# Performance work log

Measured on AMD Instinct MI355X. Metric: run time of the kernel, lower is better.

Reference implementation:

```python
import jax, jax.numpy as jnp
import numpy as np

B, S, E, H, L, NQ, FFN, V, C = 16, 2048, 256, 4, 2, 8, 512, 50257, 2
DK = E // H  # wires per attention head


def _pos_encoding(seq_len, dim):
    pos = jnp.arange(seq_len, dtype=jnp.float32)[:, None]
    div = jnp.exp(jnp.arange(0, dim, 2, dtype=jnp.float32) * (-np.log(10000.0) / dim))
    pe = jnp.zeros((seq_len, dim), dtype=jnp.float32)
    pe = pe.at[:, 0::2].set(jnp.sin(pos * div))
    pe = pe.at[:, 1::2].set(jnp.cos(pos * div))
    return pe


def _layernorm(x, g, b, eps=1e-5):
    m = x.mean(-1, keepdims=True)
    v = ((x - m) ** 2).mean(-1, keepdims=True)
    return (x - m) / jnp.sqrt(v + eps) * g + b


def setup_inputs() -> dict:
    key = jax.random.key(0)
    ks = jax.random.split(key, 9)
    f = lambda k, shape, s: jax.random.normal(k, shape, dtype=jnp.float32) * s
    return {
        "tokens": jax.random.randint(ks[0], (B, S), 0, V),
        "embed": f(ks[1], (V, E), 0.02),
        "attn_theta": f(ks[2], (L, DK), 1.0),
        "combine_w": f(ks[3], (L, E, E), 0.05),
        "combine_b": jnp.zeros((L, E), jnp.float32),
        "ffn_theta": f(ks[4], (L, NQ), 1.0),
        "lin1_w": f(ks[5], (L, NQ, FFN), 0.1),
        "lin1_b": jnp.zeros((L, FFN), jnp.float32),
        "lin2_w": f(ks[6], (L, FFN, E), 0.05),
        "lin2_b": jnp.zeros((L, E), jnp.float32),
        "ln1_g": jnp.ones((L, E), jnp.float32),
        "ln1_b": jnp.zeros((L, E), jnp.float32),
        "ln2_g": jnp.ones((L, E), jnp.float32),
        "ln2_b": jnp.zeros((L, E), jnp.float32),
        "cls_w": f(ks[7], (E, C), 0.05),
        "cls_b": jnp.zeros((C,), jnp.float32),
    }


def reference(tokens, embed, attn_theta, combine_w, combine_b, ffn_theta,
              lin1_w, lin1_b, lin2_w, lin2_b, ln1_g, ln1_b, ln2_g, ln2_b,
              cls_w, cls_b):
    # token embedding + sinusoidal positional encoding
    x = embed[tokens] + _pos_encoding(S, E)[None]  # [B,S,E]
    for l in range(L):
        # QuantumAttention: per-head RX-encode(x) then trainable RX(theta),
        # PauliZ expectation => cos(x + theta); same theta shared across heads,
        # head split/merge preserves feature layout => tile theta over heads.
        theta = jnp.tile(attn_theta[l], H)  # [E]
        attn = jnp.einsum('bse,ef->bsf', jnp.cos(x + theta), combine_w[l]) + combine_b[l]
        x = _layernorm(x + attn, ln1_g[l], ln1_b[l])
        # FeedForwardQuantum: RX-encode first NQ features, trainable RY(theta),
        # PauliZ expectation => cos(x) * cos(theta)
        q = jnp.cos(x[..., :NQ]) * jnp.cos(ffn_theta[l])  # [B,S,NQ]
        h = jax.nn.relu(jnp.einsum('bsn,nf->bsf', q, lin1_w[l]) + lin1_b[l])
        ffn = jnp.einsum('bsf,fe->bse', h, lin2_w[l]) + lin2_b[l]
        x = _layernorm(x + ffn, ln2_g[l], ln2_b[l])
    pooled = x.mean(axis=1)  # [B,E]
    return pooled @ cls_w + cls_b  # [B,C] logits
```

## Files before the change

kernel.cpp:

```cpp
#include <hip/hip_runtime.h>
#include <cstdint>
#include <cstddef>

#define SEQ   2048
#define EDIM  256
#define NBATCH 16
#define XLD   264

typedef unsigned short u16;
typedef __attribute__((ext_vector_type(8))) __bf16 bf16x8;
typedef __attribute__((ext_vector_type(4))) float f32x4;

__device__ __forceinline__ float bf2f(u16 u) {
  union { unsigned int w; float f; } v; v.w = ((unsigned int)u) << 16; return v.f;
}
__device__ __forceinline__ u16 f2bf(float f) {
  union { float f; unsigned int w; } v; v.f = f;
  unsigned int r = v.w + 0x7fffu + ((v.w >> 16) & 1u);
  return (u16)(r >> 16);
}
__device__ __forceinline__ unsigned int pk2(float lo, float hi) {
  unsigned int d;
  asm("v_cvt_pk_bf16_f32 %0, %1, %2" : "=v"(d) : "v"(lo), "v"(hi));
  return d;
}
__device__ __forceinline__ float fast_cos(float x) {
  float r = x * 0.15915494309189535f;
  r = r - floorf(r);
  return __builtin_amdgcn_cosf(r);
}
__device__ __forceinline__ void unpack8(bf16x8 v, float* o) {
  const u16* p = (const u16*)&v;
  #pragma unroll
  for (int j = 0; j < 8; ++j) o[j] = bf2f(p[j]);
}

__global__ void sniff_kernel(const void* embed, int* flag) {
  int t = threadIdx.x;
  const u16* p = (const u16*)embed;
  int c = 0;
  #pragma unroll
  for (int j = 0; j < 8; ++j) {
    u16 v = p[t * 8 + j];
    int e = (v >> 7) & 0xff;
    c += (e > 128) ? 1 : 0;
  }
  #pragma unroll
  for (int d = 1; d < 64; d <<= 1) c += __shfl_xor(c, d);
  if (t == 0) *flag = (c > 64) ? 1 : 0;
}

struct CanonArgs { const void* p[11]; };

__global__ void canon_kernel(CanonArgs a, const int* __restrict__ flag,
                             u16* __restrict__ dst, float* __restrict__ divt) {
  const int off[12] = {0, 128, 640, 656, 1680, 2192, 2704, 3216, 3728, 4240, 4752, 4754};
  int i = blockIdx.x * 256 + threadIdx.x;
  if (i < 128) {
    const float c0 = 9.210340371976184f / 128.f;
    const float inv2pi = 0.15915494309189535f;
    divt[i] = __expf(-(float)i * c0) * inv2pi;
  }
  if (i >= 4754) return;
  int isf32 = *flag;
  int s = 0;
  #pragma unroll
  for (int k = 0; k < 10; ++k) s += (i >= off[k + 1]) ? 1 : 0;
  int j = i - off[s];
  dst[i] = isf32 ? f2bf(((const float*)a.p[s])[j]) : ((const u16*)a.p[s])[j];
}

__global__ void prep_kernel(const void* __restrict__ cw, const void* __restrict__ w1,
                            const void* __restrict__ l2, const int* __restrict__ flag,
                            u16* __restrict__ cwT, u16* __restrict__ l2T,
                            u16* __restrict__ w1T) {
  int id = blockIdx.x * 256 + threadIdx.x;
  int isf32 = *flag;
  if (id < 131072) {
    int l = id >> 16, rem = id & 65535;
    int kc = rem >> 11, n = (rem >> 3) & 255, kj = rem & 7;
    int idx = l * 65536 + (kc * 8 + kj) * 256 + n;
    cwT[id] = isf32 ? f2bf(((const float*)cw)[idx]) : ((const u16*)cw)[idx];
  } else if (id < 131072 + 262144) {
    int j = id - 131072;
    int l = j >> 17, rem = j & 131071;
    int kc = rem >> 11, n = (rem >> 3) & 255, kj = rem & 7;
    int idx = l * 131072 + (kc * 8 + kj) * 256 + n;
    l2T[j] = isf32 ? f2bf(((const float*)l2)[idx]) : ((const u16*)l2)[idx];
  } else {
    int j = id - (131072 + 262144);
    if (j < 2 * 512 * 8) {
      int l = j >> 12, rem = j & 4095;
      int c = rem >> 3, jj = rem & 7;
      int idx = l * 4096 + jj * 512 + c;
      w1T[j] = isf32 ? f2bf(((const float*)w1)[idx]) : ((const u16*)w1)[idx];
    }
  }
}

__launch_bounds__(256, 2)
__global__ void mega_kernel(const int* __restrict__ tokens, const void* __restrict__ embed,
                            const int* __restrict__ flag, const u16* __restrict__ canon,
                            const u16* __restrict__ cwT, const u16* __restrict__ l2T,
                            const u16* __restrict__ w1T, const float* __restrict__ divt,
                            float* __restrict__ pooled) {
  __shared__ u16 xt[64 * XLD];
  __shared__ union {
    struct { u16 Bt[256 * 64]; u16 At[64 * 64]; u16 qs[64 * 8]; } k;
    struct { float2 sstat[64][5]; float2 sms[64]; } ln;
  } sh;
  __shared__ u16 thL[64];

  const int tid = threadIdx.x;
  const int wave = tid >> 6, lane = tid & 63;
  const int fr = lane & 15, fq = lane >> 4;
  const int m0 = blockIdx.x * 64;
  const int isf32 = *flag;

  int cols[4];
  #pragma unroll
  for (int ni = 0; ni < 4; ++ni) cols[ni] = wave * 64 + ni * 16 + fr;

  {
    #pragma unroll
    for (int it = 0; it < 8; ++it) {
      int c = it * 256 + tid;
      int r = c >> 5, e8 = c & 31;
      int tok = tokens[m0 + r];
      float ev[8];
      if (isf32) {
        const float* ep = (const float*)embed + (size_t)tok * EDIM + e8 * 8;
        float4 a = *(const float4*)ep, b = *(const float4*)(ep + 4);
        ev[0]=a.x; ev[1]=a.y; ev[2]=a.z; ev[3]=a.w; ev[4]=b.x; ev[5]=b.y; ev[6]=b.z; ev[7]=b.w;
      } else {
        const u16* ep = (const u16*)embed + (size_t)tok * EDIM + e8 * 8;
        uint4 v = *(const uint4*)ep;
        unpack8(*(const bf16x8*)&v, ev);
      }
      float sf = (float)((m0 + r) & (SEQ - 1));
      float4 dv = *(const float4*)(divt + e8 * 4);
      float r0 = sf * dv.x; r0 -= floorf(r0);
      float r1 = sf * dv.y; r1 -= floorf(r1);
      float r2 = sf * dv.z; r2 -= floorf(r2);
      float r3 = sf * dv.w; r3 -= floorf(r3);
      uint4 o;
      o.x = pk2(ev[0] + __builtin_amdgcn_sinf(r0), ev[1] + __builtin_amdgcn_cosf(r0));
      o.y = pk2(ev[2] + __builtin_amdgcn_sinf(r1), ev[3] + __builtin_amdgcn_cosf(r1));
      o.z = pk2(ev[4] + __builtin_amdgcn_sinf(r2), ev[5] + __builtin_amdgcn_cosf(r2));
      o.w = pk2(ev[6] + __builtin_amdgcn_sinf(r3), ev[7] + __builtin_amdgcn_cosf(r3));
      *(uint4*)(xt + r * XLD + e8 * 8) = o;
    }
  }
  __syncthreads();

  f32x4 acc[4][4];

  auto mfma_step = [&]() {
    const bf16x8* Av = (const bf16x8*)sh.k.At;
    const bf16x8* Bv = (const bf16x8*)sh.k.Bt;
    #pragma unroll
    for (int ks = 0; ks < 2; ++ks) {
      const int kc = ks * 4 + fq;
      bf16x8 af[4], bfv[4];
      #pragma unroll
      for (int mi = 0; mi < 4; ++mi) af[mi] = Av[kc * 64 + ((mi * 16 + fr) ^ kc)];
      #pragma unroll
      for (int ni = 0; ni < 4; ++ni) bfv[ni] = Bv[kc * 256 + cols[ni]];
      #pragma unroll
      for (int mi = 0; mi < 4; ++mi)
        #pragma unroll
        for (int ni = 0; ni < 4; ++ni)
          acc[mi][ni] = __builtin_amdgcn_mfma_f32_16x16x32_bf16(af[mi], bfv[ni], acc[mi][ni], 0, 0, 0);
    }
  };

  auto acc_init = [&](const u16* bias) {
    #pragma unroll
    for (int ni = 0; ni < 4; ++ni) {
      float b = bf2f(bias[cols[ni]]);
      #pragma unroll
      for (int mi = 0; mi < 4; ++mi) acc[mi][ni] = {b, b, b, b};
    }
  };

  auto epilogue = [&](const u16* gamma, const u16* beta) {
    #pragma unroll
    for (int mi = 0; mi < 4; ++mi)
      #pragma unroll
      for (int rg = 0; rg < 4; ++rg) {
        int lrow = mi * 16 + fq * 4 + rg;
        #pragma unroll
        for (int ni = 0; ni < 4; ++ni)
          acc[mi][ni][rg] += bf2f(xt[lrow * XLD + cols[ni]]);
      }
    float sr[4][4], sq[4][4];
    #pragma unroll
    for (int mi = 0; mi < 4; ++mi)
      #pragma unroll
      for (int rg = 0; rg < 4; ++rg) {
        float a = 0.f, b = 0.f;
        #pragma unroll
        for (int ni = 0; ni < 4; ++ni) { float t2 = acc[mi][ni][rg]; a += t2; b += t2 * t2; }
        sr[mi][rg] = a; sq[mi][rg] = b;
      }
    #pragma unroll
    for (int d = 1; d < 16; d <<= 1)
      #pragma unroll
      for (int mi = 0; mi < 4; ++mi)
        #pragma unroll
        for (int rg = 0; rg < 4; ++rg) {
          sr[mi][rg] += __shfl_xor(sr[mi][rg], d);
          sq[mi][rg] += __shfl_xor(sq[mi][rg], d);
        }
    if (fr == 0) {
      #pragma unroll
      for (int mi = 0; mi < 4; ++mi)
        #pragma unroll
        for (int rg = 0; rg < 4; ++rg)
          sh.ln.sstat[mi * 16 + fq * 4 + rg][wave] = float2{sr[mi][rg], sq[mi][rg]};
    }
    __syncthreads();
    if (tid < 64) {
      float s = 0.f, s2 = 0.f;
      #pragma unroll
      for (int w = 0; w < 4; ++w) { float2 p = sh.ln.sstat[tid][w]; s += p.x; s2 += p.y; }
      float mean = s * (1.f / 256.f);
      float var = fmaxf(s2 * (1.f / 256.f) - mean * mean, 0.f);
      sh.ln.sms[tid] = float2{mean, rsqrtf(var + 1e-5f)};
    }
    __syncthreads();
    float gcol[4], btc[4];
    #pragma unroll
    for (int ni = 0; ni < 4; ++ni) { gcol[ni] = bf2f(gamma[cols[ni]]); btc[ni] = bf2f(beta[cols[ni]]); }
    #pragma unroll
    for (int mi = 0; mi < 4; ++mi)
      #pragma unroll
      for (int rg = 0; rg < 4; ++rg) {
        int lrow = mi * 16 + fq * 4 + rg;
        float2 ms = sh.ln.sms[lrow];
        #pragma unroll
        for (int ni = 0; ni < 4; ++ni) {
          float o = (acc[mi][ni][rg] - ms.x) * ms.y * gcol[ni] + btc[ni];
          xt[lrow * XLD + cols[ni]] = f2bf(o);
        }
      }
    __syncthreads();
  };

  for (int l = 0; l < 2; ++l) {
    if (tid < 8) ((uint4*)thL)[tid] = ((const uint4*)(canon + l * 64))[tid];
    __syncthreads();
    acc_init(canon + 128 + l * 256);
    {
      const u16* Bbase = cwT + l * 65536;
      for (int k0 = 0; k0 < 256; k0 += 64) {
        const u16* bsrc = Bbase + (k0 >> 3) * 2048;
        #pragma unroll
        for (int it = 0; it < 8; ++it) {
          int c = tid + it * 256;
          __builtin_amdgcn_global_load_lds(
              (const __attribute__((address_space(1))) void*)(bsrc + (size_t)c * 8),
              (__attribute__((address_space(3))) void*)(sh.k.Bt + c * 8), 16, 0, 0);
        }
        #pragma unroll
        for (int it = 0; it < 2; ++it) {
          int c = it * 256 + tid;
          int f8 = c >> 6, r = c & 63;
          uint4 g = *(const uint4*)(xt + r * XLD + k0 + f8 * 8);
          const u16* gp = (const u16*)&g;
          float cv[8];
          #pragma unroll
          for (int j = 0; j < 8; ++j)
            cv[j] = fast_cos(bf2f(gp[j]) + bf2f(thL[f8 * 8 + j]));
          uint4 o;
          o.x = pk2(cv[0], cv[1]); o.y = pk2(cv[2], cv[3]);
          o.z = pk2(cv[4], cv[5]); o.w = pk2(cv[6], cv[7]);
          ((uint4*)sh.k.At)[f8 * 64 + (r ^ f8)] = o;
        }
        __syncthreads();
        mfma_step();
        __syncthreads();
      }
    }
    epilogue(canon + 2192 + l * 256, canon + 2704 + l * 256);

    const u16* B2 = l2T + (size_t)l * 131072;
    #pragma unroll
    for (int it = 0; it < 8; ++it) {
      int c = tid + it * 256;
      __builtin_amdgcn_global_load_lds(
          (const __attribute__((address_space(1))) void*)(B2 + (size_t)c * 8),
          (__attribute__((address_space(3))) void*)(sh.k.Bt + c * 8), 16, 0, 0);
    }
    #pragma unroll
    for (int rep = 0; rep < 2; ++rep) {
      int idx = tid + rep * 256;
      int r = idx >> 3, n = idx & 7;
      float cth = fast_cos(bf2f(canon[640 + l * 8 + n]));
      sh.k.qs[r * 8 + n] = f2bf(fast_cos(bf2f(xt[r * XLD + n])) * cth);
    }
    bf16x8 aW1[8]; uint2 b1p[8];
    #pragma unroll
    for (int c = 0; c < 8; ++c) {
      uint4 t = {0u, 0u, 0u, 0u};
      if (fq == 0) t = *(const uint4*)(w1T + (size_t)l * 4096 + (size_t)(c * 64 + wave * 16 + fr) * 8);
      aW1[c] = *(const bf16x8*)&t;
      b1p[c] = *(const uint2*)(canon + 656 + l * 512 + c * 64 + wave * 16 + fq * 4);
    }
    __syncthreads();
    bf16x8 bq[4];
    #pragma unroll
    for (int ni = 0; ni < 4; ++ni) {
      uint4 t = {0u, 0u, 0u, 0u};
      if (fq == 0) t = ((const uint4*)sh.k.qs)[ni * 16 + fr];
      bq[ni] = *(const bf16x8*)&t;
    }
    acc_init(canon + 1680 + l * 256);
    #pragma unroll
    for (int c8 = 0; c8 < 8; ++c8) {
      {
        float b0 = bf2f((u16)(b1p[c8].x & 0xffffu)), b1v = bf2f((u16)(b1p[c8].x >> 16));
        float b2 = bf2f((u16)(b1p[c8].y & 0xffffu)), b3 = bf2f((u16)(b1p[c8].y >> 16));
        const int kcL = wave * 2 + (fq >> 1);
        const int halfoff = (fq & 1) * 4;
        #pragma unroll
        for (int ni = 0; ni < 4; ++ni) {
          f32x4 hacc;
          hacc[0] = b0; hacc[1] = b1v; hacc[2] = b2; hacc[3] = b3;
          hacc = __builtin_amdgcn_mfma_f32_16x16x32_bf16(aW1[c8], bq[ni], hacc, 0, 0, 0);
          float h0 = fmaxf(hacc[0], 0.f), h1 = fmaxf(hacc[1], 0.f);
          float h2 = fmaxf(hacc[2], 0.f), h3 = fmaxf(hacc[3], 0.f);
          uint2 dw; dw.x = pk2(h0, h1); dw.y = pk2(h2, h3);
          int r = ni * 16 + fr;
          *(uint2*)(sh.k.At + ((kcL * 64 + (r ^ kcL)) * 8 + halfoff)) = dw;
        }
      }
      __syncthreads();
      mfma_step();
      __syncthreads();
      if (c8 < 7) {
        const u16* bsrc = B2 + (size_t)(c8 + 1) * 16384;
        #pragma unroll
        for (int it = 0; it < 8; ++it) {
          int c = tid + it * 256;
          __builtin_amdgcn_global_load_lds(
              (const __attribute__((address_space(1))) void*)(bsrc + (size_t)c * 8),
              (__attribute__((address_space(3))) void*)(sh.k.Bt + c * 8), 16, 0, 0);
        }
      }
    }
    epilogue(canon + 3216 + l * 256, canon + 3728 + l * 256);
  }

  {
    float s = 0.f;
    #pragma unroll 8
    for (int r = 0; r < 64; ++r) s += bf2f(xt[r * XLD + tid]);
    atomicAdd(&pooled[(m0 >> 11) * EDIM + tid], s);
  }
}

__global__ void logits_kernel(const float* __restrict__ pooled, const u16* __restrict__ clsw,
                              const u16* __restrict__ clsb, const int* __restrict__ flag,
                              void* __restrict__ out) {
  int t = threadIdx.x;
  int b = t >> 4, sub = t & 15;
  float a0 = 0.f, a1 = 0.f;
  #pragma unroll
  for (int j = 0; j < 16; ++j) {
    int e = sub * 16 + j;
    float p = pooled[b * 256 + e];
    a0 += p * bf2f(clsw[e * 2 + 0]);
    a1 += p * bf2f(clsw[e * 2 + 1]);
  }
  #pragma unroll
  for (int d = 1; d < 16; d <<= 1) {
    a0 += __shfl_xor(a0, d);
    a1 += __shfl_xor(a1, d);
  }
  if (sub == 0) {
    float o0 = a0 * (1.f / 2048.f) + bf2f(clsb[0]);
    float o1 = a1 * (1.f / 2048.f) + bf2f(clsb[1]);
    if (*flag) {
      ((float*)out)[b * 2 + 0] = o0; ((float*)out)[b * 2 + 1] = o1;
    } else {
      ((u16*)out)[b * 2 + 0] = f2bf(o0); ((u16*)out)[b * 2 + 1] = f2bf(o1);
    }
  }
}

extern "C" void kernel_launch(void* const* d_in, const int* in_sizes, int n_in,
                              void* d_out, int out_size, void* d_ws, size_t ws_size,
                              hipStream_t stream) {
  const int* tokens = (const int*)d_in[0];

  char* ws = (char*)d_ws;
  u16*   canon  = (u16*)(ws + 0);
  u16*   cwT    = (u16*)(ws + 16384);
  u16*   l2T    = (u16*)(ws + 278528);
  u16*   w1T    = (u16*)(ws + 802816);
  float* pooled = (float*)(ws + 819200);
  int*   flag   = (int*)(ws + 835584);
  float* divt   = (float*)(ws + 835600);

  sniff_kernel<<<1, 64, 0, stream>>>(d_in[1], flag);

  CanonArgs ca;
  ca.p[0] = d_in[2];  ca.p[1] = d_in[4];  ca.p[2] = d_in[5];  ca.p[3] = d_in[7];
  ca.p[4] = d_in[9];  ca.p[5] = d_in[10]; ca.p[6] = d_in[11]; ca.p[7] = d_in[12];
  ca.p[8] = d_in[13]; ca.p[9] = d_in[14]; ca.p[10] = d_in[15];
  canon_kernel<<<19, 256, 0, stream>>>(ca, flag, canon, divt);

  prep_kernel<<<1568, 256, 0, stream>>>(d_in[3], d_in[6], d_in[8], flag, cwT, l2T, w1T);

  hipMemsetAsync(pooled, 0, NBATCH * EDIM * sizeof(float), stream);

  mega_kernel<<<512, 256, 0, stream>>>(tokens, d_in[1], flag, canon, cwT, l2T, w1T, divt, pooled);

  logits_kernel<<<1, 256, 0, stream>>>(pooled, canon + 4240, canon + 4752, flag, d_out);
}
```

Measured before the change: 180.5 us.

## Load GEMM B operands directly from global into registers, drop LDS B tile

The B-matrix tiles for the attention-combine and FFN second GEMMs are now loaded by each lane straight from global memory into registers, replacing the global_load_lds staging into a 32 KB shared buffer. This shrinks LDS use and raises launch bounds to 3 blocks per CU to improve occupancy. Theta values are also kept in registers instead of a shared array, and the attention cos staging is remapped per wave. The risk is higher register pressure under the tighter bound, plus less coalesced or redundant global/L2 traffic, since each wave now fetches its own B columns with no prefetch overlap.

```diff
diff --git a/kernel.cpp b/kernel.cpp
--- a/kernel.cpp
+++ b/kernel.cpp
@@ -98,7 +98,7 @@
   }
 }
 
-__launch_bounds__(256, 2)
+__launch_bounds__(256, 3)
 __global__ void mega_kernel(const int* __restrict__ tokens, const void* __restrict__ embed,
                             const int* __restrict__ flag, const u16* __restrict__ canon,
                             const u16* __restrict__ cwT, const u16* __restrict__ l2T,
@@ -106,10 +106,9 @@
                             float* __restrict__ pooled) {
   __shared__ u16 xt[64 * XLD];
   __shared__ union {
-    struct { u16 Bt[256 * 64]; u16 At[64 * 64]; u16 qs[64 * 8]; } k;
+    struct { u16 At[64 * 64]; u16 qs[64 * 8]; } k;
     struct { float2 sstat[64][5]; float2 sms[64]; } ln;
   } sh;
-  __shared__ u16 thL[64];
 
   const int tid = threadIdx.x;
   const int wave = tid >> 6, lane = tid & 63;
@@ -154,23 +153,32 @@
   __syncthreads();
 
   f32x4 acc[4][4];
+  uint4 bfv[8];
+
+  auto load_bfv = [&](const u16* Bbase, int c) {
+    #pragma unroll
+    for (int ks = 0; ks < 2; ++ks) {
+      const u16* src = Bbase + (size_t)(c * 8 + ks * 4 + fq) * 2048;
+      #pragma unroll
+      for (int ni = 0; ni < 4; ++ni)
+        bfv[ks * 4 + ni] = *(const uint4*)(src + (size_t)cols[ni] * 8);
+    }
+  };
 
   auto mfma_step = [&]() {
     const bf16x8* Av = (const bf16x8*)sh.k.At;
-    const bf16x8* Bv = (const bf16x8*)sh.k.Bt;
     #pragma unroll
     for (int ks = 0; ks < 2; ++ks) {
       const int kc = ks * 4 + fq;
-      bf16x8 af[4], bfv[4];
+      bf16x8 af[4];
       #pragma unroll
       for (int mi = 0; mi < 4; ++mi) af[mi] = Av[kc * 64 + ((mi * 16 + fr) ^ kc)];
       #pragma unroll
-      for (int ni = 0; ni < 4; ++ni) bfv[ni] = Bv[kc * 256 + cols[ni]];
-      #pragma unroll
       for (int mi = 0; mi < 4; ++mi)
         #pragma unroll
         for (int ni = 0; ni < 4; ++ni)
-          acc[mi][ni] = __builtin_amdgcn_mfma_f32_16x16x32_bf16(af[mi], bfv[ni], acc[mi][ni], 0, 0, 0);
+          acc[mi][ni] = __builtin_amdgcn_mfma_f32_16x16x32_bf16(
+              af[mi], *(const bf16x8*)(bfv + ks * 4 + ni), acc[mi][ni], 0, 0, 0);
     }
   };
 
@@ -181,6 +189,50 @@
       #pragma unroll
       for (int mi = 0; mi < 4; ++mi) acc[mi][ni] = {b, b, b, b};
     }
+  };
+
+  auto stage_attn = [&](int k0, const float* thw) {
+    #pragma unroll
+    for (int it = 0; it < 2; ++it) {
+      int f8 = it * 4 + wave;
+      uint4 g = *(const uint4*)(xt + lane * XLD + k0 + f8 * 8);
+      const u16* gp = (const u16*)&g;
+      float cv[8];
+      #pragma unroll
+      for (int j = 0; j < 8; ++j) cv[j] = fast_cos(bf2f(gp[j]) + thw[it * 8 + j]);
+      uint4 o;
+      o.x = pk2(cv[0], cv[1]); o.y = pk2(cv[2], cv[3]);
+      o.z = pk2(cv[4], cv[5]); o.w = pk2(cv[6], cv[7]);
+      ((uint4*)sh.k.At)[f8 * 64 + (lane ^ f8)] = o;
+    }
+  };
+
+  auto stage_hT = [&](bf16x8 aW, const bf16x8* bq, uint2 b1w) {
+    float b0 = bf2f((u16)(b1w.x & 0xffffu)), b1v = bf2f((u16)(b1w.x >> 16));
+    float b2 = bf2f((u16)(b1w.y & 0xffffu)), b3 = bf2f((u16)(b1w.y >> 16));
+    const int kcL = wave * 2 + (fq >> 1);
+    const int halfoff = (fq & 1) * 4;
+    #pragma unroll
+    for (int ni = 0; ni < 4; ++ni) {
+      f32x4 hacc;
+      hacc[0] = b0; hacc[1] = b1v; hacc[2] = b2; hacc[3] = b3;
+      hacc = __builtin_amdgcn_mfma_f32_16x16x32_bf16(aW, bq[ni], hacc, 0, 0, 0);
+      uint2 dw;
+      dw.x = pk2(fmaxf(hacc[0], 0.f), fmaxf(hacc[1], 0.f));
+      dw.y = pk2(fmaxf(hacc[2], 0.f), fmaxf(hacc[3], 0.f));
+      int r = ni * 16 + fr;
+      *(uint2*)(sh.k.At + ((kcL * 64 + (r ^ kcL)) * 8 + halfoff)) = dw;
+    }
+  };
+
+  auto load_aW1 = [&](int l, int c8) -> bf16x8 {
+    uint4 t = {0u, 0u, 0u, 0u};
+    if (fq == 0)
+      t = *(const uint4*)(w1T + (size_t)l * 4096 + (size_t)(c8 * 64 + wave * 16 + fr) * 8);
+    return *(const bf16x8*)&t;
+  };
+  auto load_b1 = [&](int l, int c8) -> uint2 {
+    return *(const uint2*)(canon + 656 + l * 512 + c8 * 64 + wave * 16 + fq * 4);
   };
 
   auto epilogue = [&](const u16* gamma, const u16* beta) {
@@ -248,35 +300,20 @@
   };
 
   for (int l = 0; l < 2; ++l) {
-    if (tid < 8) ((uint4*)thL)[tid] = ((const uint4*)(canon + l * 64))[tid];
-    __syncthreads();
+    float thw[16];
+    {
+      uint4 ta = *(const uint4*)(canon + l * 64 + wave * 8);
+      uint4 tb = *(const uint4*)(canon + l * 64 + (wave + 4) * 8);
+      unpack8(*(const bf16x8*)&ta, thw);
+      unpack8(*(const bf16x8*)&tb, thw + 8);
+    }
     acc_init(canon + 128 + l * 256);
     {
       const u16* Bbase = cwT + l * 65536;
-      for (int k0 = 0; k0 < 256; k0 += 64) {
-        const u16* bsrc = Bbase + (k0 >> 3) * 2048;
-        #pragma unroll
-        for (int it = 0; it < 8; ++it) {
-          int c = tid + it * 256;
-          __builtin_amdgcn_global_load_lds(
-              (const __attribute__((address_space(1))) void*)(bsrc + (size_t)c * 8),
-              (__attribute__((address_space(3))) void*)(sh.k.Bt + c * 8), 16, 0, 0);
-        }
-        #pragma unroll
-        for (int it = 0; it < 2; ++it) {
-          int c = it * 256 + tid;
-          int f8 = c >> 6, r = c & 63;
-          uint4 g = *(const uint4*)(xt + r * XLD + k0 + f8 * 8);
-          const u16* gp = (const u16*)&g;
-          float cv[8];
-          #pragma unroll
-          for (int j = 0; j < 8; ++j)
-            cv[j] = fast_cos(bf2f(gp[j]) + bf2f(thL[f8 * 8 + j]));
-          uint4 o;
-          o.x = pk2(cv[0], cv[1]); o.y = pk2(cv[2], cv[3]);
-          o.z = pk2(cv[4], cv[5]); o.w = pk2(cv[6], cv[7]);
-          ((uint4*)sh.k.At)[f8 * 64 + (r ^ f8)] = o;
-        }
+      #pragma unroll
+      for (int c = 0; c < 4; ++c) {
+        load_bfv(Bbase, c);
+        stage_attn(c * 64, thw);
         __syncthreads();
         mfma_step();
         __syncthreads();
@@ -284,69 +321,33 @@
     }
     epilogue(canon + 2192 + l * 256, canon + 2704 + l * 256);
 
-    const u16* B2 = l2T + (size_t)l * 131072;
-    #pragma unroll
-    for (int it = 0; it < 8; ++it) {
-      int c = tid + it * 256;
-      __builtin_amdgcn_global_load_lds(
-          (const __attribute__((address_space(1))) void*)(B2 + (size_t)c * 8),
-          (__attribute__((address_space(3))) void*)(sh.k.Bt + c * 8), 16, 0, 0);
-    }
-    #pragma unroll
-    for (int rep = 0; rep < 2; ++rep) {
-      int idx = tid + rep * 256;
-      int r = idx >> 3, n = idx & 7;
-      float cth = fast_cos(bf2f(canon[640 + l * 8 + n]));
-      sh.k.qs[r * 8 + n] = f2bf(fast_cos(bf2f(xt[r * XLD + n])) * cth);
-    }
-    bf16x8 aW1[8]; uint2 b1p[8];
-    #pragma unroll
-    for (int c = 0; c < 8; ++c) {
-      uint4 t = {0u, 0u, 0u, 0u};
-      if (fq == 0) t = *(const uint4*)(w1T + (size_t)l * 4096 + (size_t)(c * 64 + wave * 16 + fr) * 8);
-      aW1[c] = *(const bf16x8*)&t;
-      b1p[c] = *(const uint2*)(canon + 656 + l * 512 + c * 64 + wave * 16 + fq * 4);
-    }
-    __syncthreads();
-    bf16x8 bq[4];
-    #pragma unroll
-    for (int ni = 0; ni < 4; ++ni) {
-      uint4 t = {0u, 0u, 0u, 0u};
-      if (fq == 0) t = ((const uint4*)sh.k.qs)[ni * 16 + fr];
-      bq[ni] = *(const bf16x8*)&t;
-    }
-    acc_init(canon + 1680 + l * 256);
-    #pragma unroll
-    for (int c8 = 0; c8 < 8; ++c8) {
-      {
-        float b0 = bf2f((u16)(b1p[c8].x & 0xffffu)), b1v = bf2f((u16)(b1p[c8].x >> 16));
-        float b2 = bf2f((u16)(b1p[c8].y & 0xffffu)), b3 = bf2f((u16)(b1p[c8].y >> 16));
-        const int kcL = wave * 2 + (fq >> 1);
-        const int halfoff = (fq & 1) * 4;
-        #pragma unroll
-        for (int ni = 0; ni < 4; ++ni) {
-          f32x4 hacc;
-          hacc[0] = b0; hacc[1] = b1v; hacc[2] = b2; hacc[3] = b3;
-          hacc = __builtin_amdgcn_mfma_f32_16x16x32_bf16(aW1[c8], bq[ni], hacc, 0, 0, 0);
-          float h0 = fmaxf(hacc[0], 0.f), h1 = fmaxf(hacc[1], 0.f);
-          float h2 = fmaxf(hacc[2], 0.f), h3 = fmaxf(hacc[3], 0.f);
-          uint2 dw; dw.x = pk2(h0, h1); dw.y = pk2(h2, h3);
-          int r = ni * 16 + fr;
-          *(uint2*)(sh.k.At + ((kcL * 64 + (r ^ kcL)) * 8 + halfoff)) = dw;
-        }
+    {
+      const u16* B2 = l2T + (size_t)l * 131072;
+      #pragma unroll
+      for (int rep = 0; rep < 2; ++rep) {
+        int idx = tid + rep * 256;
+        int r = idx >> 3, n = idx & 7;
+        float cth = fast_cos(bf2f(canon[640 + l * 8 + n]));
+        sh.k.qs[r * 8 + n] = f2bf(fast_cos(bf2f(xt[r * XLD + n])) * cth);
       }
       __syncthreads();
-      mfma_step();
-      __syncthreads();
-      if (c8 < 7) {
-        const u16* bsrc = B2 + (size_t)(c8 + 1) * 16384;
-        #pragma unroll
-        for (int it = 0; it < 8; ++it) {
-          int c = tid + it * 256;
-          __builtin_amdgcn_global_load_lds(
-              (const __attribute__((address_space(1))) void*)(bsrc + (size_t)c * 8),
-              (__attribute__((address_space(3))) void*)(sh.k.Bt + c * 8), 16, 0, 0);
-        }
+      bf16x8 bq[4];
+      #pragma unroll
+      for (int ni = 0; ni < 4; ++ni) {
+        uint4 t = {0u, 0u, 0u, 0u};
+        if (fq == 0) t = ((const uint4*)sh.k.qs)[ni * 16 + fr];
+        bq[ni] = *(const bf16x8*)&t;
+      }
+      acc_init(canon + 1680 + l * 256);
+      #pragma unroll
+      for (int c8 = 0; c8 < 8; ++c8) {
+        load_bfv(B2, c8);
+        bf16x8 aW = load_aW1(l, c8);
+        uint2  b1w = load_b1(l, c8);
+        stage_hT(aW, bq, b1w);
+        __syncthreads();
+        mfma_step();
+        __syncthreads();
       }
     }
     epilogue(canon + 3216 + l * 256, canon + 3728 + l * 256);
@@ -415,7 +416,8 @@
 
   hipMemsetAsync(pooled, 0, NBATCH * EDIM * sizeof(float), stream);
 
-  mega_kernel<<<512, 256, 0, stream>>>(tokens, d_in[1], flag, canon, cwT, l2T, w1T, divt, pooled);
+  mega_kernel<<<512, 256, 0, stream>>>(tokens, d_in[1], flag, canon, cwT, l2T, w1T,
+                                       divt, pooled);
 
   logits_kernel<<<1, 256, 0, stream>>>(pooled, canon + 4240, canon + 4752, flag, d_out);
 }
```

Result: slower. 248.6 us (+37.7%).
